# Kernel tuning notes

Measured on AMD Instinct MI355X. Metric: run time of the kernel, lower is better.

Reference implementation:

```python
import jax, jax.numpy as jnp
import numpy as np

B, N, DV = 32, 1024, 512
L, S, DT = 256, 8, 512
VOCAB = 1024
BAND = 16
LN_EPS = 1e-5


def setup_inputs() -> dict:
    key = jax.random.key(0)
    ks = jax.random.split(key, 12)
    w = lambda k, shp: jax.random.normal(k, shp, dtype=jnp.float32) * 0.02
    return {
        "vis_tokens": jax.random.normal(ks[0], (B, N, DV), dtype=jnp.float32),
        "txt_ctx_ids": jax.random.randint(ks[1], (B, L, S), 0, VOCAB, dtype=jnp.int32),
        "emb_w": w(ks[2], (VOCAB, DT)),        # embedding table, tied with classifier
        "wq": w(ks[3], (DV, DT)),              # q_proj: d_txt -> d_vis
        "wk": w(ks[4], (DV, DV)),
        "wv": w(ks[5], (DV, DV)),
        "wv2t": w(ks[6], (DT, DV)),            # vis2txt: d_vis -> d_txt
        "dw_k": w(ks[7], (DT, 1, 3)),          # depthwise conv1d kernel (O, I/g=1, K)
        "pw_k": w(ks[8], (DT, DT, 1)),         # pointwise conv1d kernel
        "ln_g": jnp.ones((DT,), jnp.float32),
        "ln_b": jnp.zeros((DT,), jnp.float32),
        "dir_alpha": jnp.float32(0.2),
    }


def reference(vis_tokens, txt_ctx_ids, emb_w, wq, wk, wv, wv2t, dw_k, pw_k, ln_g, ln_b, dir_alpha):
    b, n, dv = vis_tokens.shape
    E = emb_w[txt_ctx_ids]                       # [B, L, S, Dt]
    bl = b * E.shape[1]
    x = E.reshape(bl, E.shape[2], DT).transpose(0, 2, 1)  # [B*L, Dt, S]
    dn = ('NCH', 'OIH', 'NCH')
    h = jax.lax.conv_general_dilated(x, dw_k, (1,), 'SAME', dimension_numbers=dn,
                                     feature_group_count=DT)
    y = jax.lax.conv_general_dilated(jax.nn.silu(h), pw_k, (1,), 'SAME', dimension_numbers=dn)
    x = x + y
    m = x.mean(axis=2)                           # [B*L, Dt]
    mu = m.mean(-1, keepdims=True)
    var = ((m - mu) ** 2).mean(-1, keepdims=True)
    q_txt = ((m - mu) * jax.lax.rsqrt(var + LN_EPS) * ln_g + ln_b).reshape(b, -1, DT)  # [B, L, Dt]

    Q = q_txt @ wq.T                             # [B, L, Dv]
    K = vis_tokens @ wk.T                        # [B, N, Dv]
    V = vis_tokens @ wv.T
    logits = jnp.einsum('bld,bnd->bln', Q, K) * (dv ** -0.5)

    # linear centers (torch linspace(0, N-1, L).long() truncates toward zero)
    centers = jnp.linspace(0.0, n - 1, q_txt.shape[1]).astype(jnp.int32)  # [L]
    centers = jnp.broadcast_to(centers[None, :], (b, q_txt.shape[1]))
    idx = jnp.arange(n)[None, None, :]
    signed = (centers[..., None] - idx).astype(jnp.float32)
    logits = logits + dir_alpha * (signed / (BAND + 1e-6))
    keep = jnp.abs(idx - centers[..., None]) <= BAND
    logits = jnp.where(keep, logits, -jnp.inf)

    A = jax.nn.softmax(logits, axis=-1)          # [B, L, N]
    Fv = jnp.einsum('bln,bnd->bld', A, V)        # dropout in source is undefined attr; identity
    H = Fv @ wv2t.T                              # [B, L, Dt]
    cls = H @ emb_w.T                            # tied classifier
    return (cls, H, A)
```

## Files before the change

kernel.cpp:

```cpp
#include <hip/hip_runtime.h>
#include <cmath>

typedef unsigned short u16;
typedef __attribute__((ext_vector_type(8))) short bf16x8;
typedef __attribute__((ext_vector_type(4))) float f32x4;
typedef __attribute__((ext_vector_type(8))) unsigned short u16x8;

#define B_  32
#define N_  1024
#define L_  256
#define S_  8
#define DT_ 512
#define BAND_ 16

__device__ __forceinline__ u16 f2bf(float f) {
  union { float f; unsigned u; } x; x.f = f;
  unsigned r = (x.u + 0x7fffu + ((x.u >> 16) & 1u)) >> 16;
  return (u16)r;
}
__device__ __forceinline__ float bf2f(u16 h) {
  union { unsigned u; float f; } x; x.u = ((unsigned)h) << 16;
  return x.f;
}

__global__ __launch_bounds__(256) void cvt_bf16(
    const float* __restrict__ in, u16* __restrict__ out, int n4) {
  int i = blockIdx.x * 256 + threadIdx.x;
  if (i < n4) {
    float4 v = ((const float4*)in)[i];
    ushort4 o;
    o.x = f2bf(v.x); o.y = f2bf(v.y); o.z = f2bf(v.z); o.w = f2bf(v.w);
    ((ushort4*)out)[i] = o;
  }
}

__global__ __launch_bounds__(256) void cvt_weights(
    const float* __restrict__ e, const float* __restrict__ q,
    const float* __restrict__ k, const float* __restrict__ v,
    const float* __restrict__ t, const float* __restrict__ pw,
    u16* __restrict__ eo, u16* __restrict__ qo, u16* __restrict__ kvo,
    u16* __restrict__ to, u16* __restrict__ po) {
  int i = blockIdx.x * 256 + threadIdx.x;
  const float* src; u16* dst; int soff, doff;
  if (i < 131072)      { src = e;  dst = eo;  soff = i;          doff = soff; }
  else if (i < 196608) { src = q;  dst = qo;  soff = i - 131072; doff = soff; }
  else if (i < 262144) { src = k;  dst = kvo; soff = i - 196608; doff = soff; }
  else if (i < 327680) { src = v;  dst = kvo; soff = i - 262144; doff = soff + 65536; }
  else if (i < 393216) { src = t;  dst = to;  soff = i - 327680; doff = soff; }
  else                 { src = pw; dst = po;  soff = i - 393216; doff = soff; }
  float4 vv = ((const float4*)src)[soff];
  ushort4 o;
  o.x = f2bf(vv.x); o.y = f2bf(vv.y); o.z = f2bf(vv.z); o.w = f2bf(vv.w);
  ((ushort4*)dst)[doff] = o;
}

__global__ __launch_bounds__(256) void text_front(
    const int* __restrict__ ids, const float* __restrict__ emb,
    const float* __restrict__ dwk, u16* __restrict__ shm,
    float* __restrict__ mbuf) {
  int bl = blockIdx.x;
  int tid = threadIdx.x;
  __shared__ int sid[S_];
  if (tid < S_) sid[tid] = ids[bl * S_ + tid];
  __syncthreads();
  for (int c = tid; c < DT_; c += 256) {
    float x[S_];
#pragma unroll
    for (int s = 0; s < S_; ++s) x[s] = emb[(size_t)sid[s] * DT_ + c];
    float k0 = dwk[c * 3 + 0], k1 = dwk[c * 3 + 1], k2 = dwk[c * 3 + 2];
    float me = 0.f, sh = 0.f;
#pragma unroll
    for (int s = 0; s < S_; ++s) {
      float xm = (s > 0) ? x[s - 1] : 0.0f;
      float xp = (s < S_ - 1) ? x[s + 1] : 0.0f;
      float h = k0 * xm + k1 * x[s] + k2 * xp;
      float si = h / (1.0f + expf(-h));
      me += x[s];
      sh += si;
    }
    shm[(size_t)bl * DT_ + c] = f2bf(sh * (1.0f / S_));
    mbuf[(size_t)bl * DT_ + c] = me * (1.0f / S_);
  }
}

template <bool ACC, bool WF32, bool WBF16>
__global__ __launch_bounds__(256) void gemm_mfma(
    const u16* __restrict__ A, const u16* __restrict__ B,
    float* __restrict__ C, u16* __restrict__ Cb, int M, int N, int K) {
  __shared__ u16 As[8192];
  __shared__ u16 Bs[8192];
  const int tid = threadIdx.x;
  const int w = tid >> 6;
  const int lane = tid & 63;

  const int gx = gridDim.x;
  const int bid = blockIdx.y * gx + blockIdx.x;
  const int nwg = gx * gridDim.y;
  const int logical = (bid & 7) * (nwg >> 3) + (bid >> 3);
  const int bm = (logical / gx) << 7;
  const int bn = (logical % gx) << 7;
  const int wr = w >> 1, wc = w & 1;

  const int r0 = (w << 4) + (lane >> 2);
  const int kc = (lane & 3) << 3;
  const u16* Ag0 = A + (size_t)(bm + r0) * K + kc;
  const u16* Ag1 = Ag0 + (size_t)64 * K;
  const u16* Bg0 = B + (size_t)(bn + r0) * K + kc;
  const u16* Bg1 = Bg0 + (size_t)64 * K;

  int aoff[4], boff[4];
#pragma unroll
  for (int m = 0; m < 4; ++m)
    aoff[m] = (((wr << 6) + (m << 4) + (lane & 15)) << 5) + ((lane >> 4) << 3);
#pragma unroll
  for (int n = 0; n < 4; ++n)
    boff[n] = (((wc << 6) + (n << 4) + (lane & 15)) << 5) + ((lane >> 4) << 3);

  f32x4 acc[4][4];
#pragma unroll
  for (int m = 0; m < 4; ++m)
#pragma unroll
    for (int n = 0; n < 4; ++n) acc[m][n] = (f32x4){0.f, 0.f, 0.f, 0.f};

#define STAGE(buf, kt)                                                        \
  {                                                                           \
    u16* as_ = As + (buf) * 4096 + (w << 9);                                  \
    u16* bs_ = Bs + (buf) * 4096 + (w << 9);                                  \
    __builtin_amdgcn_global_load_lds(                                         \
        (const __attribute__((address_space(1))) void*)(Ag0 + (kt)),          \
        (__attribute__((address_space(3))) void*)as_, 16, 0, 0);              \
    __builtin_amdgcn_global_load_lds(                                         \
        (const __attribute__((address_space(1))) void*)(Ag1 + (kt)),          \
        (__attribute__((address_space(3))) void*)(as_ + 2048), 16, 0, 0);     \
    __builtin_amdgcn_global_load_lds(                                         \
        (const __attribute__((address_space(1))) void*)(Bg0 + (kt)),          \
        (__attribute__((address_space(3))) void*)bs_, 16, 0, 0);              \
    __builtin_amdgcn_global_load_lds(                                         \
        (const __attribute__((address_space(1))) void*)(Bg1 + (kt)),          \
        (__attribute__((address_space(3))) void*)(bs_ + 2048), 16, 0, 0);     \
  }

  const int nt = K >> 5;
  STAGE(0, 0);
  __syncthreads();
  int cur = 0;
  for (int t = 0; t < nt; ++t) {
    if (t + 1 < nt) STAGE(cur ^ 1, (t + 1) << 5);
    const u16* Ab = As + cur * 4096;
    const u16* Bb = Bs + cur * 4096;
    bf16x8 af[4], bfr[4];
#pragma unroll
    for (int m = 0; m < 4; ++m) af[m] = *(const bf16x8*)(Ab + aoff[m]);
#pragma unroll
    for (int n = 0; n < 4; ++n) bfr[n] = *(const bf16x8*)(Bb + boff[n]);
#pragma unroll
    for (int m = 0; m < 4; ++m)
#pragma unroll
      for (int n = 0; n < 4; ++n)
        acc[m][n] = __builtin_amdgcn_mfma_f32_16x16x32_bf16(
            af[m], bfr[n], acc[m][n], 0, 0, 0);
    __syncthreads();
    cur ^= 1;
  }
#undef STAGE

  const int rb = bm + (wr << 6) + ((lane >> 4) << 2);
  const int cb = bn + (wc << 6) + (lane & 15);
#pragma unroll
  for (int m = 0; m < 4; ++m) {
#pragma unroll
    for (int n = 0; n < 4; ++n) {
      int col = cb + (n << 4);
#pragma unroll
      for (int j = 0; j < 4; ++j) {
        size_t idx = (size_t)(rb + (m << 4) + j) * N + col;
        float v = acc[m][n][j];
        if (ACC) v += C[idx];
        if (WF32) C[idx] = v;
        if (WBF16) Cb[idx] = f2bf(v);
      }
    }
  }
}

__global__ __launch_bounds__(256) void ln_kernel(
    const float* __restrict__ m, const float* __restrict__ g,
    const float* __restrict__ bta, u16* __restrict__ q) {
  int row = blockIdx.x;
  int tid = threadIdx.x;
  float v0 = m[(size_t)row * 512 + tid];
  float v1 = m[(size_t)row * 512 + 256 + tid];
  __shared__ float red[4], red2[4];
  float s = v0 + v1;
#pragma unroll
  for (int d = 32; d; d >>= 1) s += __shfl_xor(s, d);
  if ((tid & 63) == 0) red[tid >> 6] = s;
  __syncthreads();
  float mu = (red[0] + red[1] + red[2] + red[3]) * (1.0f / 512.0f);
  float d0 = v0 - mu, d1 = v1 - mu;
  float s2 = d0 * d0 + d1 * d1;
#pragma unroll
  for (int d = 32; d; d >>= 1) s2 += __shfl_xor(s2, d);
  if ((tid & 63) == 0) red2[tid >> 6] = s2;
  __syncthreads();
  float var = (red2[0] + red2[1] + red2[2] + red2[3]) * (1.0f / 512.0f);
  float r = rsqrtf(var + 1e-5f);
  q[(size_t)row * 512 + tid] = f2bf(d0 * r * g[tid] + bta[tid]);
  q[(size_t)row * 512 + 256 + tid] = f2bf(d1 * r * g[tid + 256] + bta[tid + 256]);
}

__global__ __launch_bounds__(512) void attn_kernel(
    const u16* __restrict__ Qb, const u16* __restrict__ KV,
    const float* __restrict__ alpha_p, float* __restrict__ A,
    u16* __restrict__ Fv) {
  __shared__ u16 KV_s[96 * 512];
  __shared__ u16 Q_s[16 * 520];
  __shared__ float S_s[16 * 100];

  const int bid = blockIdx.x;
  const int logical = (bid & 7) * 64 + (bid >> 3);
  const int b = logical >> 4, lg = logical & 15;
  const int l0 = lg * 16;
  const int tid = threadIdx.x;
  const int w = tid >> 6, lane = tid & 63;
  const float al = *alpha_p;

  const int c_min = (1023 * l0) / 255;
  const int kb0 = min(max(c_min - BAND_, 0), N_ - 96);

  {
    const size_t rowb = (size_t)(b * N_ + kb0);
    for (int rr = 0; rr < 12; ++rr) {
      const int r = w * 12 + rr;
      const u16* src = KV + (rowb + r) * 1024 + ((lane * 8) ^ ((r & 7) << 3));
      u16* dst = KV_s + r * 512;
      __builtin_amdgcn_global_load_lds(
          (const __attribute__((address_space(1))) void*)src,
          (__attribute__((address_space(3))) void*)dst, 16, 0, 0);
    }
  }
  {
    const int r = tid >> 5;
    const u16* qrow = Qb + (size_t)(b * L_ + l0 + r) * 512;
#pragma unroll
    for (int h = 0; h < 2; ++h) {
      const int ch = (tid & 31) + h * 32;
      u16x8 v = *(const u16x8*)(qrow + ch * 8);
      *(u16x8*)(Q_s + r * 520 + ch * 8) = v;
    }
  }
  __syncthreads();

  if (w < 6) {
    f32x4 acc = {0.f, 0.f, 0.f, 0.f};
    const int arow = (lane & 15) * 520 + ((lane >> 4) << 3);
    const int key = w * 16 + (lane & 15);
    const int swz = (key & 7) << 3;
    for (int ks = 0; ks < 16; ++ks) {
      bf16x8 aq = *(const bf16x8*)(Q_s + arow + ks * 32);
      bf16x8 bk =
          *(const bf16x8*)(KV_s + key * 512 + ((ks * 32 + ((lane >> 4) << 3)) ^ swz));
      acc = __builtin_amdgcn_mfma_f32_16x16x32_bf16(aq, bk, acc, 0, 0, 0);
    }
#pragma unroll
    for (int j = 0; j < 4; ++j)
      S_s[((lane >> 4) * 4 + j) * 100 + w * 16 + (lane & 15)] = acc[j];
  }
  __syncthreads();

  {
    const size_t rowb = (size_t)(b * N_ + kb0);
    for (int rr = 0; rr < 12; ++rr) {
      const int r = w * 12 + rr;
      const u16* src =
          KV + (rowb + r) * 1024 + 512 + ((lane * 8) ^ ((r & 7) << 3));
      u16* dst = KV_s + r * 512;
      __builtin_amdgcn_global_load_lds(
          (const __attribute__((address_space(1))) void*)src,
          (__attribute__((address_space(3))) void*)dst, 16, 0, 0);
    }
  }

#pragma unroll
  for (int rr = 0; rr < 2; ++rr) {
    const int l = 2 * w + rr;
    const int c = (1023 * (l0 + l)) / 255;
    const int g0 = kb0 + lane, g1 = kb0 + 64 + lane;
    const bool v0 = (g0 >= c - BAND_) && (g0 <= c + BAND_);
    const bool v1 = (lane < 32) && (g1 >= c - BAND_) && (g1 <= c + BAND_);
    const float sc = 0.044194173824159216f;
    float x0 = v0 ? S_s[l * 100 + lane] * sc +
                        al * ((float)(c - g0) * (1.0f / 16.000001f))
                  : -INFINITY;
    float x1 = v1 ? S_s[l * 100 + 64 + lane] * sc +
                        al * ((float)(c - g1) * (1.0f / 16.000001f))
                  : -INFINITY;
    float mx = fmaxf(x0, x1);
#pragma unroll
    for (int d = 32; d; d >>= 1) mx = fmaxf(mx, __shfl_xor(mx, d));
    float e0 = v0 ? expf(x0 - mx) : 0.0f;
    float e1 = v1 ? expf(x1 - mx) : 0.0f;
    float sm = e0 + e1;
#pragma unroll
    for (int d = 32; d; d >>= 1) sm += __shfl_xor(sm, d);
    const float inv = 1.0f / sm;
    S_s[l * 100 + lane] = e0 * inv;
    if (lane < 32) S_s[l * 100 + 64 + lane] = e1 * inv;
    const int lo = max(0, c - BAND_), hi = min(N_ - 1, c + BAND_);
    float* Arow = A + (size_t)(b * L_ + l0 + l) * N_;
#pragma unroll
    for (int p4 = 0; p4 < 4; ++p4) {
      const int p = (p4 * 64 + lane) * 4;
      float4 v;
      v.x = (p + 0 >= lo && p + 0 <= hi) ? S_s[l * 100 + p + 0 - kb0] : 0.0f;
      v.y = (p + 1 >= lo && p + 1 <= hi) ? S_s[l * 100 + p + 1 - kb0] : 0.0f;
      v.z = (p + 2 >= lo && p + 2 <= hi) ? S_s[l * 100 + p + 2 - kb0] : 0.0f;
      v.w = (p + 3 >= lo && p + 3 <= hi) ? S_s[l * 100 + p + 3 - kb0] : 0.0f;
      ((float4*)Arow)[p4 * 64 + lane] = v;
    }
  }
  __syncthreads();

#pragma unroll
  for (int rr = 0; rr < 2; ++rr) {
    const int l = 2 * w + rr;
    const int c = (1023 * (l0 + l)) / 255;
    const int jlo = max(0, c - BAND_) - kb0, jhi = min(N_ - 1, c + BAND_) - kb0;
    float acc[8] = {};
    for (int j = jlo; j <= jhi; ++j) {
      const float avj = S_s[l * 100 + j];
      const u16x8 v =
          *(const u16x8*)(KV_s + j * 512 + ((lane * 8) ^ ((j & 7) << 3)));
#pragma unroll
      for (int t = 0; t < 8; ++t) acc[t] += avj * bf2f(v[t]);
    }
    u16x8 fo;
#pragma unroll
    for (int t = 0; t < 8; ++t) fo[t] = f2bf(acc[t]);
    *(u16x8*)(Fv + (size_t)(b * L_ + l0 + l) * 512 + lane * 8) = fo;
  }
}

extern "C" void kernel_launch(void* const* d_in, const int* in_sizes, int n_in,
                              void* d_out, int out_size, void* d_ws,
                              size_t ws_size, hipStream_t stream) {
  const float* vis = (const float*)d_in[0];
  const int* ids = (const int*)d_in[1];
  const float* emb = (const float*)d_in[2];
  const float* wq = (const float*)d_in[3];
  const float* wk = (const float*)d_in[4];
  const float* wvp = (const float*)d_in[5];
  const float* wv2t = (const float*)d_in[6];
  const float* dwk = (const float*)d_in[7];
  const float* pwk = (const float*)d_in[8];
  const float* lng = (const float*)d_in[9];
  const float* lnb = (const float*)d_in[10];
  const float* alpha = (const float*)d_in[11];

  float* out_cls = (float*)d_out;
  float* out_H = out_cls + (size_t)8192 * 1024;
  float* out_A = out_H + (size_t)8192 * 512;

  char* p = (char*)d_ws;
  u16* visb = (u16*)p;              p += (size_t)32768 * 512 * 2;
  u16* KVb  = (u16*)p;              p += (size_t)32768 * 1024 * 2;
  u16* embb = (u16*)p;              p += (size_t)1024 * 512 * 2;
  u16* wqb  = (u16*)p;              p += (size_t)512 * 512 * 2;
  u16* wkvb = (u16*)p;              p += (size_t)1024 * 512 * 2;
  u16* wv2tb= (u16*)p;              p += (size_t)512 * 512 * 2;
  u16* pwkb = (u16*)p;              p += (size_t)512 * 512 * 2;
  u16* shmb = (u16*)p;              p += (size_t)8192 * 512 * 2;
  float* mbuf = (float*)p;          p += (size_t)8192 * 512 * 4;
  u16* qbuf = (u16*)p;              p += (size_t)8192 * 512 * 2;
  u16* Qbf  = (u16*)p;              p += (size_t)8192 * 512 * 2;
  u16* Fvb  = (u16*)p;              p += (size_t)8192 * 512 * 2;
  u16* Hb   = (u16*)p;              p += (size_t)8192 * 512 * 2;

  cvt_bf16<<<16384, 256, 0, stream>>>(vis, visb, 32768 * 512 / 4);
  cvt_weights<<<1792, 256, 0, stream>>>(emb, wq, wk, wvp, wv2t, pwk,
                                        embb, wqb, wkvb, wv2tb, pwkb);

  gemm_mfma<false, false, true><<<dim3(8, 256), 256, 0, stream>>>(
      visb, wkvb, nullptr, KVb, 32768, 1024, 512);

  text_front<<<8192, 256, 0, stream>>>(ids, emb, dwk, shmb, mbuf);
  gemm_mfma<true, true, false><<<dim3(4, 64), 256, 0, stream>>>(
      shmb, pwkb, mbuf, nullptr, 8192, 512, 512);
  ln_kernel<<<8192, 256, 0, stream>>>(mbuf, lng, lnb, qbuf);
  gemm_mfma<false, false, true><<<dim3(4, 64), 256, 0, stream>>>(
      qbuf, wqb, nullptr, Qbf, 8192, 512, 512);
  attn_kernel<<<512, 512, 0, stream>>>(Qbf, KVb, alpha, out_A, Fvb);
  gemm_mfma<false, true, true><<<dim3(4, 64), 256, 0, stream>>>(
      Fvb, wv2tb, out_H, Hb, 8192, 512, 512);
  gemm_mfma<false, true, false><<<dim3(8, 64), 256, 0, stream>>>(
      Hb, embb, out_cls, nullptr, 8192, 1024, 512);
}
```

Before: 219.6 us.

## Fuse vis fp32-to-bf16 conversion into KV GEMM and add 128x64 tile GEMM

The separate pass that converts vis_tokens to bf16 is removed. A new KV projection GEMM now loads fp32 A tiles through registers, converts them with packed bf16 conversion instructions and writes them to LDS, while B is still staged with direct global-to-LDS loads. This avoids writing and re-reading a 32 MB bf16 copy of vis. The three 8192x512 GEMMs move to a 128x64 tile variant with twice as many workgroups, to fill more compute units; the cost is more A re-reads and possibly lower per-block efficiency.

```diff
diff --git a/kernel.cpp b/kernel.cpp
--- a/kernel.cpp
+++ b/kernel.cpp
@@ -22,16 +22,10 @@
   union { unsigned u; float f; } x; x.u = ((unsigned)h) << 16;
   return x.f;
 }
-
-__global__ __launch_bounds__(256) void cvt_bf16(
-    const float* __restrict__ in, u16* __restrict__ out, int n4) {
-  int i = blockIdx.x * 256 + threadIdx.x;
-  if (i < n4) {
-    float4 v = ((const float4*)in)[i];
-    ushort4 o;
-    o.x = f2bf(v.x); o.y = f2bf(v.y); o.z = f2bf(v.z); o.w = f2bf(v.w);
-    ((ushort4*)out)[i] = o;
-  }
+__device__ __forceinline__ unsigned cvtpk(float lo, float hi) {
+  unsigned r;
+  asm volatile("v_cvt_pk_bf16_f32 %0, %1, %2" : "=v"(r) : "v"(lo), "v"(hi));
+  return r;
 }
 
 __global__ __launch_bounds__(256) void cvt_weights(
@@ -83,6 +77,123 @@
   }
 }
 
+__global__ __launch_bounds__(256) void gemm_kv_f32a(
+    const float* __restrict__ A, const u16* __restrict__ B,
+    u16* __restrict__ Cb, int M, int N, int K) {
+  __shared__ u16 As[8192];
+  __shared__ u16 Bs[8192];
+  const int tid = threadIdx.x;
+  const int w = tid >> 6;
+  const int lane = tid & 63;
+
+  const int gx = gridDim.x;
+  const int bid = blockIdx.y * gx + blockIdx.x;
+  const int nwg = gx * gridDim.y;
+  const int logical = (bid & 7) * (nwg >> 3) + (bid >> 3);
+  const int bm = (logical / gx) << 7;
+  const int bn = (logical % gx) << 7;
+  const int wr = w >> 1, wc = w & 1;
+
+  const int arow = tid >> 1;
+  const int ahalf = (tid & 1) << 4;
+  const float* Ap = A + (size_t)(bm + arow) * K + ahalf;
+  const int awoff = arow * 32 + ahalf;
+
+  const int r0 = (w << 4) + (lane >> 2);
+  const int kc = (lane & 3) << 3;
+  const u16* Bg0 = B + (size_t)(bn + r0) * K + kc;
+  const u16* Bg1 = Bg0 + (size_t)64 * K;
+
+  int aoff[4], boff[4];
+#pragma unroll
+  for (int m = 0; m < 4; ++m)
+    aoff[m] = (((wr << 6) + (m << 4) + (lane & 15)) << 5) + ((lane >> 4) << 3);
+#pragma unroll
+  for (int n = 0; n < 4; ++n)
+    boff[n] = (((wc << 6) + (n << 4) + (lane & 15)) << 5) + ((lane >> 4) << 3);
+
+  f32x4 acc[4][4];
+#pragma unroll
+  for (int m = 0; m < 4; ++m)
+#pragma unroll
+    for (int n = 0; n < 4; ++n) acc[m][n] = (f32x4){0.f, 0.f, 0.f, 0.f};
+
+  float4 ar0, ar1, ar2, ar3;
+#define LOADA(kt)                              \
+  {                                            \
+    ar0 = *(const float4*)(Ap + (kt));         \
+    ar1 = *(const float4*)(Ap + (kt) + 4);     \
+    ar2 = *(const float4*)(Ap + (kt) + 8);     \
+    ar3 = *(const float4*)(Ap + (kt) + 12);    \
+  }
+#define WRITEA(buf)                                              \
+  {                                                              \
+    uint4 q0, q1;                                                \
+    q0.x = cvtpk(ar0.x, ar0.y); q0.y = cvtpk(ar0.z, ar0.w);      \
+    q0.z = cvtpk(ar1.x, ar1.y); q0.w = cvtpk(ar1.z, ar1.w);      \
+    q1.x = cvtpk(ar2.x, ar2.y); q1.y = cvtpk(ar2.z, ar2.w);      \
+    q1.z = cvtpk(ar3.x, ar3.y); q1.w = cvtpk(ar3.z, ar3.w);      \
+    *(uint4*)(As + (buf) * 4096 + awoff) = q0;                   \
+    *(uint4*)(As + (buf) * 4096 + awoff + 8) = q1;               \
+  }
+#define STAGEB(buf, kt)                                                       \
+  {                                                                           \
+    u16* bs_ = Bs + (buf) * 4096 + (w << 9);                                  \
+    __builtin_amdgcn_global_load_lds(                                         \
+        (const __attribute__((address_space(1))) void*)(Bg0 + (kt)),          \
+        (__attribute__((address_space(3))) void*)bs_, 16, 0, 0);              \
+    __builtin_amdgcn_global_load_lds(                                         \
+        (const __attribute__((address_space(1))) void*)(Bg1 + (kt)),          \
+        (__attribute__((address_space(3))) void*)(bs_ + 2048), 16, 0, 0);     \
+  }
+
+  const int nt = K >> 5;
+  LOADA(0);
+  STAGEB(0, 0);
+  WRITEA(0);
+  __syncthreads();
+  int cur = 0;
+  for (int t = 0; t < nt; ++t) {
+    if (t + 1 < nt) LOADA((t + 1) << 5);
+    const u16* Ab = As + cur * 4096;
+    const u16* Bb = Bs + cur * 4096;
+    bf16x8 af[4], bfr[4];
+#pragma unroll
+    for (int m = 0; m < 4; ++m) af[m] = *(const bf16x8*)(Ab + aoff[m]);
+#pragma unroll
+    for (int n = 0; n < 4; ++n) bfr[n] = *(const bf16x8*)(Bb + boff[n]);
+#pragma unroll
+    for (int m = 0; m < 4; ++m)
+#pragma unroll
+      for (int n = 0; n < 4; ++n)
+        acc[m][n] = __builtin_amdgcn_mfma_f32_16x16x32_bf16(
+            af[m], bfr[n], acc[m][n], 0, 0, 0);
+    if (t + 1 < nt) {
+      WRITEA(cur ^ 1);
+      STAGEB(cur ^ 1, (t + 1) << 5);
+    }
+    __syncthreads();
+    cur ^= 1;
+  }
+#undef LOADA
+#undef WRITEA
+#undef STAGEB
+
+  const int rb = bm + (wr << 6) + ((lane >> 4) << 2);
+  const int cb = bn + (wc << 6) + (lane & 15);
+#pragma unroll
+  for (int m = 0; m < 4; ++m)
+#pragma unroll
+    for (int n = 0; n < 4; ++n) {
+      int col = cb + (n << 4);
+#pragma unroll
+      for (int j = 0; j < 4; ++j) {
+        size_t idx = (size_t)(rb + (m << 4) + j) * N + col;
+        Cb[idx] = f2bf(acc[m][n][j]);
+      }
+    }
+}
+
 template <bool ACC, bool WF32, bool WBF16>
 __global__ __launch_bounds__(256) void gemm_mfma(
     const u16* __restrict__ A, const u16* __restrict__ B,
@@ -167,7 +278,7 @@
   const int rb = bm + (wr << 6) + ((lane >> 4) << 2);
   const int cb = bn + (wc << 6) + (lane & 15);
 #pragma unroll
-  for (int m = 0; m < 4; ++m) {
+  for (int m = 0; m < 4; ++m)
 #pragma unroll
     for (int n = 0; n < 4; ++n) {
       int col = cb + (n << 4);
@@ -180,7 +291,100 @@
         if (WBF16) Cb[idx] = f2bf(v);
       }
     }
-  }
+}
+
+template <bool ACC, bool WF32, bool WBF16>
+__global__ __launch_bounds__(256) void gemm_n64(
+    const u16* __restrict__ A, const u16* __restrict__ B,
+    float* __restrict__ C, u16* __restrict__ Cb, int M, int N, int K) {
+  __shared__ u16 As[8192];
+  __shared__ u16 Bs[4096];
+  const int tid = threadIdx.x;
+  const int w = tid >> 6;
+  const int lane = tid & 63;
+
+  const int gx = gridDim.x;
+  const int bid = blockIdx.y * gx + blockIdx.x;
+  const int nwg = gx * gridDim.y;
+  const int logical = (bid & 7) * (nwg >> 3) + (bid >> 3);
+  const int bm = (logical / gx) << 7;
+  const int bn = (logical % gx) << 6;
+
+  const int r0 = (w << 4) + (lane >> 2);
+  const int kc = (lane & 3) << 3;
+  const u16* Ag0 = A + (size_t)(bm + r0) * K + kc;
+  const u16* Ag1 = Ag0 + (size_t)64 * K;
+  const u16* Bg0 = B + (size_t)(bn + r0) * K + kc;
+
+  int aoff[2], boff[4];
+#pragma unroll
+  for (int m = 0; m < 2; ++m)
+    aoff[m] = (((w << 5) + (m << 4) + (lane & 15)) << 5) + ((lane >> 4) << 3);
+#pragma unroll
+  for (int n = 0; n < 4; ++n)
+    boff[n] = (((n << 4) + (lane & 15)) << 5) + ((lane >> 4) << 3);
+
+  f32x4 acc[2][4];
+#pragma unroll
+  for (int m = 0; m < 2; ++m)
+#pragma unroll
+    for (int n = 0; n < 4; ++n) acc[m][n] = (f32x4){0.f, 0.f, 0.f, 0.f};
+
+#define STAGE(buf, kt)                                                        \
+  {                                                                           \
+    u16* as_ = As + (buf) * 4096 + (w << 9);                                  \
+    u16* bs_ = Bs + (buf) * 2048 + (w << 9);                                  \
+    __builtin_amdgcn_global_load_lds(                                         \
+        (const __attribute__((address_space(1))) void*)(Ag0 + (kt)),          \
+        (__attribute__((address_space(3))) void*)as_, 16, 0, 0);              \
+    __builtin_amdgcn_global_load_lds(                                         \
+        (const __attribute__((address_space(1))) void*)(Ag1 + (kt)),          \
+        (__attribute__((address_space(3))) void*)(as_ + 2048), 16, 0, 0);     \
+    __builtin_amdgcn_global_load_lds(                                         \
+        (const __attribute__((address_space(1))) void*)(Bg0 + (kt)),          \
+        (__attribute__((address_space(3))) void*)bs_, 16, 0, 0);              \
+  }
+
+  const int nt = K >> 5;
+  STAGE(0, 0);
+  __syncthreads();
+  int cur = 0;
+  for (int t = 0; t < nt; ++t) {
+    if (t + 1 < nt) STAGE(cur ^ 1, (t + 1) << 5);
+    const u16* Ab = As + cur * 4096;
+    const u16* Bb = Bs + cur * 2048;
+    bf16x8 af[2], bfr[4];
+#pragma unroll
+    for (int m = 0; m < 2; ++m) af[m] = *(const bf16x8*)(Ab + aoff[m]);
+#pragma unroll
+    for (int n = 0; n < 4; ++n) bfr[n] = *(const bf16x8*)(Bb + boff[n]);
+#pragma unroll
+    for (int m = 0; m < 2; ++m)
+#pragma unroll
+      for (int n = 0; n < 4; ++n)
+        acc[m][n] = __builtin_amdgcn_mfma_f32_16x16x32_bf16(
+            af[m], bfr[n], acc[m][n], 0, 0, 0);
+    __syncthreads();
+    cur ^= 1;
+  }
+#undef STAGE
+
+  const int rb = bm + (w << 5) + ((lane >> 4) << 2);
+  const int cb = bn + (lane & 15);
+#pragma unroll
+  for (int m = 0; m < 2; ++m)
+#pragma unroll
+    for (int n = 0; n < 4; ++n) {
+      int col = cb + (n << 4);
+#pragma unroll
+      for (int j = 0; j < 4; ++j) {
+        size_t idx = (size_t)(rb + (m << 4) + j) * N + col;
+        float v = acc[m][n][j];
+        if (ACC) v += C[idx];
+        if (WF32) C[idx] = v;
+        if (WBF16) Cb[idx] = f2bf(v);
+      }
+    }
 }
 
 __global__ __launch_bounds__(256) void ln_kernel(
@@ -362,7 +566,6 @@
   float* out_A = out_H + (size_t)8192 * 512;
 
   char* p = (char*)d_ws;
-  u16* visb = (u16*)p;              p += (size_t)32768 * 512 * 2;
   u16* KVb  = (u16*)p;              p += (size_t)32768 * 1024 * 2;
   u16* embb = (u16*)p;              p += (size_t)1024 * 512 * 2;
   u16* wqb  = (u16*)p;              p += (size_t)512 * 512 * 2;
@@ -376,21 +579,20 @@
   u16* Fvb  = (u16*)p;              p += (size_t)8192 * 512 * 2;
   u16* Hb   = (u16*)p;              p += (size_t)8192 * 512 * 2;
 
-  cvt_bf16<<<16384, 256, 0, stream>>>(vis, visb, 32768 * 512 / 4);
   cvt_weights<<<1792, 256, 0, stream>>>(emb, wq, wk, wvp, wv2t, pwk,
                                         embb, wqb, wkvb, wv2tb, pwkb);
 
-  gemm_mfma<false, false, true><<<dim3(8, 256), 256, 0, stream>>>(
-      visb, wkvb, nullptr, KVb, 32768, 1024, 512);
+  gemm_kv_f32a<<<dim3(8, 256), 256, 0, stream>>>(
+      vis, wkvb, KVb, 32768, 1024, 512);
 
   text_front<<<8192, 256, 0, stream>>>(ids, emb, dwk, shmb, mbuf);
-  gemm_mfma<true, true, false><<<dim3(4, 64), 256, 0, stream>>>(
+  gemm_n64<true, true, false><<<dim3(8, 64), 256, 0, stream>>>(
       shmb, pwkb, mbuf, nullptr, 8192, 512, 512);
   ln_kernel<<<8192, 256, 0, stream>>>(mbuf, lng, lnb, qbuf);
-  gemm_mfma<false, false, true><<<dim3(4, 64), 256, 0, stream>>>(
+  gemm_n64<false, false, true><<<dim3(8, 64), 256, 0, stream>>>(
       qbuf, wqb, nullptr, Qbf, 8192, 512, 512);
   attn_kernel<<<512, 512, 0, stream>>>(Qbf, KVb, alpha, out_A, Fvb);
-  gemm_mfma<false, true, true><<<dim3(4, 64), 256, 0, stream>>>(
+  gemm_n64<false, true, true><<<dim3(8, 64), 256, 0, stream>>>(
       Fvb, wv2tb, out_H, Hb, 8192, 512, 512);
   gemm_mfma<false, true, false><<<dim3(8, 64), 256, 0, stream>>>(
       Hb, embb, out_cls, nullptr, 8192, 1024, 512);
```

Result: slower. 224.2 us (+2.1%).
